# Optimization experiments

Measured on AMD Instinct MI355X. Metric: run time of the kernel, lower is better.

## Reference

```python
import jax, jax.numpy as jnp
import numpy as np

B, S, D, H, O, E, TOPK = 4, 2048, 512, 1024, 512, 8, 2


def setup_inputs() -> dict:
    key = jax.random.key(0)
    ks = jax.random.split(key, 6)
    s = lambda d: 1.0 / np.sqrt(d)
    return {
        "x": jax.random.normal(ks[0], (B, S, D), dtype=jnp.float32),
        "Wg": jax.random.normal(ks[1], (D, E), dtype=jnp.float32) * s(D),
        "W1": jax.random.normal(ks[2], (E, D, H), dtype=jnp.float32) * s(D),
        "b1": jnp.zeros((E, H), dtype=jnp.float32),
        "W2": jax.random.normal(ks[3], (E, H, O), dtype=jnp.float32) * s(H),
        "b2": jnp.zeros((E, O), dtype=jnp.float32),
    }


def reference(x, Wg, W1, b1, W2, b2):
    Bsz, Seq, Din = x.shape
    T = Bsz * Seq
    xm = x.reshape(T, Din)                       # [T, D] token matrix
    # router: softmax over experts, then top-k (ProbabilitySamplerTopk)
    probs = jax.nn.softmax(xm @ Wg, axis=-1)     # [T, E]
    top_p, top_i = jax.lax.top_k(probs, TOPK)    # [T, k]
    # dense scattered gates (topKProbabilitiesScattered in _computeGating);
    # zero entries for non-selected experts make the einsum combine exactly
    # equal to the original gather->per-expert-GEMM->index_add pipeline.
    gates = jnp.zeros((T, E), dtype=probs.dtype).at[
        jnp.arange(T)[:, None], top_i
    ].set(top_p)                                 # [T, E]
    # per-expert 2-layer MLP (inputExperts -> activation -> outputExperts)
    h = jax.nn.gelu(jnp.einsum("td,edh->teh", xm, W1) + b1[None])  # [T, E, H]
    y = jnp.einsum("teh,eho->teo", h, W2) + b2[None]               # [T, E, O]
    # weighted combine (multiply_by_gates + index_add)
    out = jnp.einsum("te,teo->to", gates, y)     # [T, O]
    return out.reshape(Bsz, Seq, O)
```

## Files before the change

### kernel.cpp

```cpp
#include <hip/hip_runtime.h>

#define T_TOK 8192
#define DIM   512
#define HID   1024
#define OUTD  512
#define NE    8

typedef __attribute__((ext_vector_type(8))) short short8v;
typedef __attribute__((ext_vector_type(4))) float f32x4;

__device__ __forceinline__ unsigned short f2bf(float f) {
  unsigned int u = __builtin_bit_cast(unsigned int, f);
  u += 0x7fffu + ((u >> 16) & 1u);
  return (unsigned short)(u >> 16);
}

__device__ __forceinline__ float bf2f(unsigned short h) {
  unsigned int u = ((unsigned int)h) << 16;
  return __builtin_bit_cast(float, u);
}

__device__ __forceinline__ void gload_lds16(const void* g, void* l) {
  __builtin_amdgcn_global_load_lds(
      (__attribute__((address_space(1))) void*)g,
      (__attribute__((address_space(3))) void*)l, 16, 0, 0);
}

__device__ __forceinline__ float gelu_f(float v) {
  const float c0 = 0.7978845608028654f;
  float u = c0 * (v + 0.044715f * v * v * v);
  return v / (1.0f + __expf(-2.0f * u));
}

__global__ __launch_bounds__(256) void k_trans_all(
    const float* __restrict__ W1, const float* __restrict__ W2,
    unsigned short* __restrict__ W1t, unsigned short* __restrict__ W2t) {
  __shared__ float tile[32][33];
  int bid = blockIdx.x;
  int which = bid >> 12;
  int r = bid & 4095;
  int e = r >> 9;
  int t = r & 511;
  int R = which ? HID : DIM;
  int C = which ? OUTD : HID;
  int tx, ty;
  if (which == 0) { ty = t >> 5; tx = t & 31; }
  else            { ty = t >> 4; tx = t & 15; }
  const float* inE = (which ? W2 : W1) + (size_t)e * R * C;
  unsigned short* outE = (which ? W2t : W1t) + (size_t)e * R * C;
  int c0 = tx * 32, r0 = ty * 32;
  int x = threadIdx.x, y = threadIdx.y;
#pragma unroll
  for (int i = 0; i < 32; i += 8)
    tile[y + i][x] = inE[(size_t)(r0 + y + i) * C + (c0 + x)];
  __syncthreads();
#pragma unroll
  for (int i = 0; i < 32; i += 8)
    outE[(size_t)(c0 + y + i) * R + (r0 + x)] = f2bf(tile[x][y + i]);
}

__global__ __launch_bounds__(256) void k_router(
    const float* __restrict__ x, const float* __restrict__ Wg,
    int* __restrict__ top_e, float* __restrict__ top_p) {
  int lane = threadIdx.x & 63;
  int t = blockIdx.x * 4 + (threadIdx.x >> 6);
  const float* xr = x + (size_t)t * DIM;
  int j0 = lane * 8;
  float4 xa = *(const float4*)(xr + j0);
  float4 xb = *(const float4*)(xr + j0 + 4);
  float xl[8] = {xa.x, xa.y, xa.z, xa.w, xb.x, xb.y, xb.z, xb.w};
  float acc[8] = {0.f,0.f,0.f,0.f,0.f,0.f,0.f,0.f};
#pragma unroll
  for (int jj = 0; jj < 8; ++jj) {
    float4 w0 = *(const float4*)(Wg + (size_t)(j0 + jj) * NE);
    float4 w1 = *(const float4*)(Wg + (size_t)(j0 + jj) * NE + 4);
    acc[0] += xl[jj] * w0.x; acc[1] += xl[jj] * w0.y;
    acc[2] += xl[jj] * w0.z; acc[3] += xl[jj] * w0.w;
    acc[4] += xl[jj] * w1.x; acc[5] += xl[jj] * w1.y;
    acc[6] += xl[jj] * w1.z; acc[7] += xl[jj] * w1.w;
  }
#pragma unroll
  for (int off = 32; off >= 1; off >>= 1) {
#pragma unroll
    for (int e2 = 0; e2 < 8; ++e2) acc[e2] += __shfl_xor(acc[e2], off, 64);
  }
  if (lane == 0) {
    float m = acc[0];
#pragma unroll
    for (int e2 = 1; e2 < 8; ++e2) m = fmaxf(m, acc[e2]);
    float p[8]; float s = 0.f;
#pragma unroll
    for (int e2 = 0; e2 < 8; ++e2) { p[e2] = expf(acc[e2] - m); s += p[e2]; }
    float inv = 1.f / s;
    int i0 = 0;
#pragma unroll
    for (int e2 = 1; e2 < 8; ++e2) if (p[e2] > p[i0]) i0 = e2;
    int i1 = (i0 == 0) ? 1 : 0;
#pragma unroll
    for (int e2 = 0; e2 < 8; ++e2) if (e2 != i0 && p[e2] > p[i1]) i1 = e2;
    top_e[t * 2] = i0;  top_e[t * 2 + 1] = i1;
    top_p[t * 2] = p[i0] * inv;  top_p[t * 2 + 1] = p[i1] * inv;
  }
}

__global__ __launch_bounds__(256) void k_plan(
    const int* __restrict__ top_e, int* __restrict__ localRank,
    int* __restrict__ blockCounts) {
  __shared__ int cnt[4][NE];
  __shared__ int wbase[4][NE];
  int tid = threadIdx.x, lane = tid & 63, w = tid >> 6;
  int a = blockIdx.x * 256 + tid;
  int e = top_e[a];
  int rank = 0;
#pragma unroll
  for (int e2 = 0; e2 < NE; ++e2) {
    unsigned long long m = __ballot(e == e2);
    if (e == e2) rank = __popcll(m & ((1ULL << lane) - 1ULL));
    if (lane == 0) cnt[w][e2] = __popcll(m);
  }
  __syncthreads();
  if (tid < NE) {
    int s = 0;
#pragma unroll
    for (int w2 = 0; w2 < 4; ++w2) { wbase[w2][tid] = s; s += cnt[w2][tid]; }
    blockCounts[blockIdx.x * NE + tid] = s;
  }
  __syncthreads();
  localRank[a] = wbase[w][e] + rank;
}

__global__ void k_scan2(const int* __restrict__ blockCounts, int* __restrict__ baseBlk,
                        int* __restrict__ offs, int nBlocks) {
  __shared__ int tot[NE];
  int tid = threadIdx.x;
  if (tid < NE) {
    int s = 0;
    for (int b = 0; b < nBlocks; ++b) { baseBlk[b * NE + tid] = s; s += blockCounts[b * NE + tid]; }
    tot[tid] = s;
  }
  __syncthreads();
  if (tid == 0) {
    int s = 0;
    for (int e = 0; e < NE; ++e) { offs[e] = s; s += tot[e]; }
    offs[NE] = s;
  }
}

__global__ __launch_bounds__(256) void k_scatter(
    const float* __restrict__ x, const int* __restrict__ top_e,
    const int* __restrict__ localRank, const int* __restrict__ baseBlk,
    const int* __restrict__ offs, int* __restrict__ pos_of,
    unsigned short* __restrict__ Xp) {
  int lane = threadIdx.x & 63;
  int a = blockIdx.x * 4 + (threadIdx.x >> 6);
  int t = a >> 1;
  int e = top_e[a];
  int pos = offs[e] + baseBlk[(a >> 8) * NE + e] + localRank[a];
  if (lane == 0) pos_of[a] = pos;
  const float* xr = x + (size_t)t * DIM + lane * 8;
  float4 xa = *(const float4*)xr;
  float4 xb = *(const float4*)(xr + 4);
  short8v pk;
  pk[0] = (short)f2bf(xa.x); pk[1] = (short)f2bf(xa.y);
  pk[2] = (short)f2bf(xa.z); pk[3] = (short)f2bf(xa.w);
  pk[4] = (short)f2bf(xb.x); pk[5] = (short)f2bf(xb.y);
  pk[6] = (short)f2bf(xb.z); pk[7] = (short)f2bf(xb.w);
  *(short8v*)(Xp + (size_t)pos * DIM + lane * 8) = pk;
}

#define MFMA1(d, a, b) d = __builtin_amdgcn_mfma_f32_16x16x32_bf16(a, b, d, 0, 0, 0)

template<int NX, int LOG2NX, int EPI>
__global__ __launch_bounds__(256, 4) void k_gemm_x(
    const unsigned short* __restrict__ A,
    const unsigned short* __restrict__ Bt,
    const float* __restrict__ bias,
    const int* __restrict__ offs,
    unsigned short* __restrict__ Hout, unsigned short* __restrict__ Ybf,
    int K, int N) {
  __shared__ __align__(16) unsigned short Al[128 * 64];
  __shared__ __align__(16) unsigned short Bl[128 * 64];

  const int e = blockIdx.x & 7;
  const int slot = blockIdx.x >> 3;
  const int nSlots = gridDim.x >> 3;
  const int rowBeg = offs[e], rowEnd = offs[e + 1];
  if (rowBeg >= rowEnd) return;
  const int nMT = (rowEnd - rowBeg + 127) >> 7;
  const int nWork = nMT << LOG2NX;
  const unsigned short* Be = Bt + (size_t)e * N * K;

  const int tid = threadIdx.x, lane = tid & 63, w = tid >> 6;
  const int wr = w >> 1, wc = w & 1;
  const int fr = lane & 15, fq = lane >> 4;
  const int sRow = tid >> 3;
  const int sCe = ((((tid & 7) << 4) ^ ((sRow & 7) << 4)) >> 1);
  const int NT = K >> 6;

  for (int idx = slot; idx < nWork; idx += nSlots) {
    const int mt = idx >> LOG2NX;
    const int xb = idx & (NX - 1);
    const int m0 = rowBeg + mt * 128;
    const int n0 = xb * 128;

    const char* aP[4]; const char* bP[4];
#pragma unroll
    for (int c_ = 0; c_ < 4; ++c_) {
      int ar_ = m0 + c_ * 32 + sRow; if (ar_ > rowEnd - 1) ar_ = rowEnd - 1;
      aP[c_] = (const char*)(A + (size_t)ar_ * K + sCe);
      int br_ = n0 + c_ * 32 + sRow;
      bP[c_] = (const char*)(Be + (size_t)br_ * K + sCe);
    }

    f32x4 acc[4][4];
#pragma unroll
    for (int m = 0; m < 4; ++m)
#pragma unroll
      for (int n = 0; n < 4; ++n) acc[m][n] = (f32x4){0.f, 0.f, 0.f, 0.f};

    for (int t = 0; t < NT; ++t) {
      const int tOff = t << 7;
#pragma unroll
      for (int c_ = 0; c_ < 4; ++c_)
        gload_lds16(aP[c_] + tOff, (char*)&Al[0] + c_ * 4096 + (w << 10));
#pragma unroll
      for (int c_ = 0; c_ < 4; ++c_)
        gload_lds16(bP[c_] + tOff, (char*)&Bl[0] + c_ * 4096 + (w << 10));
      __syncthreads();
#pragma unroll
      for (int kk = 0; kk < 2; ++kk) {
        short8v av[4], bv[4];
#pragma unroll
        for (int m = 0; m < 4; ++m) {
          int row_ = wr * 64 + m * 16 + fr;
          av[m] = *(const short8v*)((const char*)&Al[0] + row_ * 128 +
                    (((kk << 6) + (fq << 4)) ^ ((fr & 7) << 4)));
        }
#pragma unroll
        for (int n = 0; n < 4; ++n) {
          int row_ = wc * 64 + n * 16 + fr;
          bv[n] = *(const short8v*)((const char*)&Bl[0] + row_ * 128 +
                    (((kk << 6) + (fq << 4)) ^ ((fr & 7) << 4)));
        }
#pragma unroll
        for (int m = 0; m < 4; ++m)
#pragma unroll
          for (int n = 0; n < 4; ++n)
            MFMA1(acc[m][n], av[m], bv[n]);
      }
      __syncthreads();
    }

#pragma unroll
    for (int m = 0; m < 4; ++m) {
#pragma unroll
      for (int j = 0; j < 4; ++j) {
        int row = m0 + wr * 64 + m * 16 + fq * 4 + j;
        if (row >= rowEnd) continue;
#pragma unroll
        for (int n = 0; n < 4; ++n) {
          int col = n0 + wc * 64 + n * 16 + fr;
          float v = acc[m][n][j] + bias[(size_t)e * N + col];
          if (EPI == 0) Hout[(size_t)row * N + col] = f2bf(gelu_f(v));
          else          Ybf[(size_t)row * N + col] = f2bf(v);
        }
      }
    }
  }
}

__global__ __launch_bounds__(256) void k_combine(
    const unsigned short* __restrict__ Y, const int* __restrict__ pos_of,
    const float* __restrict__ top_p, float* __restrict__ out) {
  int lane = threadIdx.x & 63;
  int t = blockIdx.x * 4 + (threadIdx.x >> 6);
  int p0 = pos_of[t * 2], p1 = pos_of[t * 2 + 1];
  float g0 = top_p[t * 2], g1 = top_p[t * 2 + 1];
  short8v ya = *(const short8v*)(Y + (size_t)p0 * OUTD + lane * 8);
  short8v yb = *(const short8v*)(Y + (size_t)p1 * OUTD + lane * 8);
  float4 r0, r1;
  r0.x = g0 * bf2f((unsigned short)ya[0]) + g1 * bf2f((unsigned short)yb[0]);
  r0.y = g0 * bf2f((unsigned short)ya[1]) + g1 * bf2f((unsigned short)yb[1]);
  r0.z = g0 * bf2f((unsigned short)ya[2]) + g1 * bf2f((unsigned short)yb[2]);
  r0.w = g0 * bf2f((unsigned short)ya[3]) + g1 * bf2f((unsigned short)yb[3]);
  r1.x = g0 * bf2f((unsigned short)ya[4]) + g1 * bf2f((unsigned short)yb[4]);
  r1.y = g0 * bf2f((unsigned short)ya[5]) + g1 * bf2f((unsigned short)yb[5]);
  r1.z = g0 * bf2f((unsigned short)ya[6]) + g1 * bf2f((unsigned short)yb[6]);
  r1.w = g0 * bf2f((unsigned short)ya[7]) + g1 * bf2f((unsigned short)yb[7]);
  float4* o = (float4*)(out + (size_t)t * OUTD + lane * 8);
  o[0] = r0; o[1] = r1;
}

extern "C" void kernel_launch(void* const* d_in, const int* in_sizes, int n_in,
                              void* d_out, int out_size, void* d_ws, size_t ws_size,
                              hipStream_t stream) {
  const float* x  = (const float*)d_in[0];
  const float* Wg = (const float*)d_in[1];
  const float* W1 = (const float*)d_in[2];
  const float* b1 = (const float*)d_in[3];
  const float* W2 = (const float*)d_in[4];
  const float* b2 = (const float*)d_in[5];
  float* out = (float*)d_out;

  char* p = (char*)d_ws;
  auto take = [&](size_t bytes) { char* r = p; p += (bytes + 255) & ~(size_t)255; return r; };
  unsigned short* W1t = (unsigned short*)take((size_t)NE * DIM * HID * 2);
  unsigned short* W2t = (unsigned short*)take((size_t)NE * HID * OUTD * 2);
  unsigned short* Xp  = (unsigned short*)take((size_t)2 * T_TOK * DIM * 2);
  unsigned short* Hb  = (unsigned short*)take((size_t)2 * T_TOK * HID * 2);
  unsigned short* Yb  = (unsigned short*)take((size_t)2 * T_TOK * OUTD * 2);
  int* offs   = (int*)take(4096);
  int*   top_e  = (int*)take((size_t)2 * T_TOK * 4);
  float* top_pv = (float*)take((size_t)2 * T_TOK * 4);
  int*   pos_of = (int*)take((size_t)2 * T_TOK * 4);
  int* localRank   = (int*)take((size_t)2 * T_TOK * 4);
  int* blockCounts = (int*)take((size_t)64 * NE * 4);
  int* baseBlk     = (int*)take((size_t)64 * NE * 4);

  const int PLAN_BLOCKS = (2 * T_TOK) / 256;

  k_trans_all<<<8192, dim3(32, 8), 0, stream>>>(W1, W2, W1t, W2t);
  k_router<<<T_TOK / 4, 256, 0, stream>>>(x, Wg, top_e, top_pv);
  k_plan<<<PLAN_BLOCKS, 256, 0, stream>>>(top_e, localRank, blockCounts);
  k_scan2<<<1, 64, 0, stream>>>(blockCounts, baseBlk, offs, PLAN_BLOCKS);
  k_scatter<<<(2 * T_TOK) / 4, 256, 0, stream>>>(x, top_e, localRank, baseBlk, offs, pos_of, Xp);
  k_gemm_x<8, 3, 0><<<1024, 256, 0, stream>>>(Xp, W1t, b1, offs, Hb, nullptr, DIM, HID);
  k_gemm_x<4, 2, 1><<<512, 256, 0, stream>>>(Hb, W2t, b2, offs, nullptr, Yb, HID, OUTD);
  k_combine<<<T_TOK / 4, 256, 0, stream>>>(Yb, pos_of, top_pv, out);
}
```

Baseline: 132.8 us.

## Double-buffer LDS tiles in expert GEMM with K=32 stages and compile-time K

Restructures the expert GEMM main loop to use two LDS buffers holding K=32 slices. The next slice's global-to-LDS loads are issued before computing on the current slice, with a single explicit waitcnt plus barrier per step instead of two __syncthreads. This aims to overlap memory latency with MFMA work. K also becomes a template constant and the swizzle is adapted to 64-byte rows. The trade-off is twice as many loop iterations with a smaller MFMA batch per barrier, and a full vmcnt(0) wait each step that may limit overlap.

```diff
diff --git a/kernel.cpp b/kernel.cpp
--- a/kernel.cpp
+++ b/kernel.cpp
@@ -168,18 +168,24 @@
   *(short8v*)(Xp + (size_t)pos * DIM + lane * 8) = pk;
 }
 
+#define TILE_SYNC() do {                                                      \
+    asm volatile("s_waitcnt vmcnt(0) lgkmcnt(0)" ::: "memory");               \
+    __builtin_amdgcn_sched_barrier(0);                                        \
+    __builtin_amdgcn_s_barrier();                                             \
+    __builtin_amdgcn_sched_barrier(0);                                        \
+  } while (0)
 #define MFMA1(d, a, b) d = __builtin_amdgcn_mfma_f32_16x16x32_bf16(a, b, d, 0, 0, 0)
 
-template<int NX, int LOG2NX, int EPI>
+template<int NX, int LOG2NX, int EPI, int KC>
 __global__ __launch_bounds__(256, 4) void k_gemm_x(
     const unsigned short* __restrict__ A,
     const unsigned short* __restrict__ Bt,
     const float* __restrict__ bias,
     const int* __restrict__ offs,
     unsigned short* __restrict__ Hout, unsigned short* __restrict__ Ybf,
-    int K, int N) {
-  __shared__ __align__(16) unsigned short Al[128 * 64];
-  __shared__ __align__(16) unsigned short Bl[128 * 64];
+    int N) {
+  __shared__ __align__(16) unsigned short Al[2][128 * 32];
+  __shared__ __align__(16) unsigned short Bl[2][128 * 32];
 
   const int e = blockIdx.x & 7;
   const int slot = blockIdx.x >> 3;
@@ -188,14 +194,43 @@
   if (rowBeg >= rowEnd) return;
   const int nMT = (rowEnd - rowBeg + 127) >> 7;
   const int nWork = nMT << LOG2NX;
-  const unsigned short* Be = Bt + (size_t)e * N * K;
+  const unsigned short* Be = Bt + (size_t)e * N * KC;
 
   const int tid = threadIdx.x, lane = tid & 63, w = tid >> 6;
   const int wr = w >> 1, wc = w & 1;
   const int fr = lane & 15, fq = lane >> 4;
-  const int sRow = tid >> 3;
-  const int sCe = ((((tid & 7) << 4) ^ ((sRow & 7) << 4)) >> 1);
-  const int NT = K >> 6;
+  const int sR = tid >> 2;
+  const int sCe = ((((tid & 3) << 4) ^ ((sR & 3) << 4)) >> 1);
+  constexpr int NT = KC >> 5;
+
+#define STAGE(pb2, tk) do {                                                   \
+    const int _o = (tk) << 6;                   \
+    gload_lds16(aP0 + _o, (char*)&Al[pb2][0] + (w << 10));                    \
+    gload_lds16(aP1 + _o, (char*)&Al[pb2][0] + 4096 + (w << 10));             \
+    gload_lds16(bP0 + _o, (char*)&Bl[pb2][0] + (w << 10));                    \
+    gload_lds16(bP1 + _o, (char*)&Bl[pb2][0] + 4096 + (w << 10));             \
+  } while (0)
+
+#define COMPUTE(pb2) do {                                                     \
+    short8v av[4], bv[4];                                                     \
+    _Pragma("unroll")                                                         \
+    for (int m_ = 0; m_ < 4; ++m_) {                                          \
+      int row_ = wr * 64 + m_ * 16 + fr;                                      \
+      av[m_] = *(const short8v*)((const char*)&Al[pb2][0] + row_ * 64 +       \
+                 ((fq << 4) ^ ((row_ & 3) << 4)));                            \
+    }                                                                         \
+    _Pragma("unroll")                                                         \
+    for (int n_ = 0; n_ < 4; ++n_) {                                          \
+      int row_ = wc * 64 + n_ * 16 + fr;                                      \
+      bv[n_] = *(const short8v*)((const char*)&Bl[pb2][0] + row_ * 64 +       \
+                 ((fq << 4) ^ ((row_ & 3) << 4)));                            \
+    }                                                                         \
+    _Pragma("unroll")                                                         \
+    for (int m_ = 0; m_ < 4; ++m_)                                            \
+      _Pragma("unroll")                                                       \
+      for (int n_ = 0; n_ < 4; ++n_)                                          \
+        MFMA1(acc[m_][n_], av[m_], bv[n_]);                                   \
+  } while (0)
 
   for (int idx = slot; idx < nWork; idx += nSlots) {
     const int mt = idx >> LOG2NX;
@@ -203,14 +238,12 @@
     const int m0 = rowBeg + mt * 128;
     const int n0 = xb * 128;
 
-    const char* aP[4]; const char* bP[4];
-#pragma unroll
-    for (int c_ = 0; c_ < 4; ++c_) {
-      int ar_ = m0 + c_ * 32 + sRow; if (ar_ > rowEnd - 1) ar_ = rowEnd - 1;
-      aP[c_] = (const char*)(A + (size_t)ar_ * K + sCe);
-      int br_ = n0 + c_ * 32 + sRow;
-      bP[c_] = (const char*)(Be + (size_t)br_ * K + sCe);
-    }
+    int ar0 = m0 + sR;       if (ar0 > rowEnd - 1) ar0 = rowEnd - 1;
+    int ar1 = m0 + 64 + sR;  if (ar1 > rowEnd - 1) ar1 = rowEnd - 1;
+    const char* aP0 = (const char*)(A + (size_t)ar0 * KC + sCe);
+    const char* aP1 = (const char*)(A + (size_t)ar1 * KC + sCe);
+    const char* bP0 = (const char*)(Be + (size_t)(n0 + sR) * KC + sCe);
+    const char* bP1 = (const char*)(Be + (size_t)(n0 + 64 + sR) * KC + sCe);
 
     f32x4 acc[4][4];
 #pragma unroll
@@ -218,37 +251,13 @@
 #pragma unroll
       for (int n = 0; n < 4; ++n) acc[m][n] = (f32x4){0.f, 0.f, 0.f, 0.f};
 
+    STAGE(0, 0);
+    TILE_SYNC();
     for (int t = 0; t < NT; ++t) {
-      const int tOff = t << 7;
-#pragma unroll
-      for (int c_ = 0; c_ < 4; ++c_)
-        gload_lds16(aP[c_] + tOff, (char*)&Al[0] + c_ * 4096 + (w << 10));
-#pragma unroll
-      for (int c_ = 0; c_ < 4; ++c_)
-        gload_lds16(bP[c_] + tOff, (char*)&Bl[0] + c_ * 4096 + (w << 10));
-      __syncthreads();
-#pragma unroll
-      for (int kk = 0; kk < 2; ++kk) {
-        short8v av[4], bv[4];
-#pragma unroll
-        for (int m = 0; m < 4; ++m) {
-          int row_ = wr * 64 + m * 16 + fr;
-          av[m] = *(const short8v*)((const char*)&Al[0] + row_ * 128 +
-                    (((kk << 6) + (fq << 4)) ^ ((fr & 7) << 4)));
-        }
-#pragma unroll
-        for (int n = 0; n < 4; ++n) {
-          int row_ = wc * 64 + n * 16 + fr;
-          bv[n] = *(const short8v*)((const char*)&Bl[0] + row_ * 128 +
-                    (((kk << 6) + (fq << 4)) ^ ((fr & 7) << 4)));
-        }
-#pragma unroll
-        for (int m = 0; m < 4; ++m)
-#pragma unroll
-          for (int n = 0; n < 4; ++n)
-            MFMA1(acc[m][n], av[m], bv[n]);
-      }
-      __syncthreads();
+      const int pb = t & 1;
+      if (t + 1 < NT) STAGE(pb ^ 1, t + 1);
+      COMPUTE(pb);
+      TILE_SYNC();
     }
 
 #pragma unroll
@@ -267,6 +276,8 @@
       }
     }
   }
+#undef STAGE
+#undef COMPUTE
 }
 
 __global__ __launch_bounds__(256) void k_combine(
@@ -324,7 +335,7 @@
   k_plan<<<PLAN_BLOCKS, 256, 0, stream>>>(top_e, localRank, blockCounts);
   k_scan2<<<1, 64, 0, stream>>>(blockCounts, baseBlk, offs, PLAN_BLOCKS);
   k_scatter<<<(2 * T_TOK) / 4, 256, 0, stream>>>(x, top_e, localRank, baseBlk, offs, pos_of, Xp);
-  k_gemm_x<8, 3, 0><<<1024, 256, 0, stream>>>(Xp, W1t, b1, offs, Hb, nullptr, DIM, HID);
-  k_gemm_x<4, 2, 1><<<512, 256, 0, stream>>>(Hb, W2t, b2, offs, nullptr, Yb, HID, OUTD);
+  k_gemm_x<8, 3, 0, DIM><<<1024, 256, 0, stream>>>(Xp, W1t, b1, offs, Hb, nullptr, HID);
+  k_gemm_x<4, 2, 1, HID><<<512, 256, 0, stream>>>(Hb, W2t, b2, offs, nullptr, Yb, OUTD);
   k_combine<<<T_TOK / 4, 256, 0, stream>>>(Yb, pos_of, top_pv, out);
 }
```

After: 144.8 us. 9.0% more time.
